# Optimization experiments

Hardware: AMD Instinct MI355X
Metric: run time of the kernel (lower is better)

The kernel has to match this reference:

```python
import jax, jax.numpy as jnp
import numpy as np

EMBED = 1024
HEADS = 16
HEAD_DIM = EMBED // HEADS


def setup_inputs() -> dict:
    key = jax.random.key(0)
    ks = jax.random.split(key, 5)
    x = jax.random.normal(ks[0], (4, 2048, EMBED), dtype=jnp.float32)
    s = 1.0 / np.sqrt(EMBED)
    W_qkv = jax.random.normal(ks[1], (EMBED, 3 * EMBED), dtype=jnp.float32) * s
    b_qkv = jnp.zeros((3 * EMBED,), dtype=jnp.float32)
    W_proj = jax.random.normal(ks[2], (EMBED, EMBED), dtype=jnp.float32) * s
    b_proj = jnp.zeros((EMBED,), dtype=jnp.float32)
    return {"x": x, "W_qkv": W_qkv, "b_qkv": b_qkv, "W_proj": W_proj, "b_proj": b_proj}


def reference(x, W_qkv, b_qkv, W_proj, b_proj):
    B, S, E = x.shape
    scale = 1.0 / np.sqrt(HEAD_DIM)
    qkv = x @ W_qkv + b_qkv                      # [B,S,3E]
    qkv = qkv.reshape(B, S, 3, HEADS, HEAD_DIM)
    q, k, v = qkv[:, :, 0], qkv[:, :, 1], qkv[:, :, 2]   # [B,S,H,D]
    scores = jnp.einsum('bshd,bthd->bhst', q, k) * scale  # [B,H,S,S]
    attn = jax.nn.softmax(scores, axis=-1)
    out = jnp.einsum('bhst,bthd->bshd', attn, v)          # [B,S,H,D]
    out = out.reshape(B, S, E)
    return out @ W_proj + b_proj
```

## Files before the change

kernel.cpp:

```cpp
#include <hip/hip_runtime.h>
#include <math.h>

#define EMBED 1024
#define HEADS 16
#define HD    64
#define SEQ   2048
#define BATCH 4
#define ROWS  (BATCH * SEQ)

typedef _Float16 f16;
typedef __attribute__((ext_vector_type(8))) _Float16 f16x8;
typedef __attribute__((ext_vector_type(4))) _Float16 f16x4;
typedef __attribute__((ext_vector_type(2))) _Float16 f16x2;
typedef __attribute__((ext_vector_type(4))) float    fx4;

typedef __attribute__((address_space(3))) char  lds_char;
typedef __attribute__((address_space(1))) const char glb_char;

#define SCALE_Q 0.18033688011112042f

__global__ __launch_bounds__(256) void prep(const float* __restrict__ x,
                                            f16* __restrict__ x_h,
                                            const float* __restrict__ Wqkv,
                                            f16* __restrict__ Wqt,
                                            const float* __restrict__ Wproj,
                                            f16* __restrict__ Wpt) {
    const int blk = blockIdx.x;
    if (blk < 8192) {
        const int i = (blk * 256 + threadIdx.x) * 4;
        const float4 v = *(const float4*)(x + i);
        f16x4 o = {(f16)v.x, (f16)v.y, (f16)v.z, (f16)v.w};
        *(f16x4*)(x_h + i) = o;
        return;
    }
    __shared__ float t[32][33];
    const float* W;
    f16* Wt;
    int N, bx, by;
    if (blk < 8192 + 3072) {
        const int b2 = blk - 8192;
        W = Wqkv; Wt = Wqt; N = 3072; bx = b2 % 96; by = b2 / 96;
    } else {
        const int b2 = blk - 8192 - 3072;
        W = Wproj; Wt = Wpt; N = 1024; bx = b2 % 32; by = b2 / 32;
    }
    const int tx = threadIdx.x & 31, ty = threadIdx.x >> 5;
    const int k0 = by * 32, n0 = bx * 32;
    #pragma unroll
    for (int i = 0; i < 4; i++)
        t[ty + i * 8][tx] = W[(size_t)(k0 + ty + i * 8) * N + n0 + tx];
    __syncthreads();
    #pragma unroll
    for (int i = 0; i < 4; i++)
        Wt[(size_t)(n0 + ty + i * 8) * 1024 + k0 + tx] = (f16)t[tx][ty + i * 8];
}

template <int MODE>
__global__ __launch_bounds__(256) void gemm_f16k(const f16* __restrict__ A,
                                                 const f16* __restrict__ Bt,
                                                 const float* __restrict__ bias,
                                                 float* __restrict__ Cf,
                                                 f16* __restrict__ qH,
                                                 f16* __restrict__ kH,
                                                 f16* __restrict__ vT,
                                                 int M, int N, int K) {
    __shared__ alignas(16) f16 As[128][64];
    __shared__ alignas(16) f16 Bs[128][64];
    const int tid  = threadIdx.x;
    const int wave = tid >> 6;
    const int lane = tid & 63;
    const int quad = lane >> 4;
    const int l16  = lane & 15;

    const int nwg  = gridDim.x * gridDim.y;
    const int flat = blockIdx.y * gridDim.x + blockIdx.x;
    const int swz  = (flat & 7) * (nwg >> 3) + (flat >> 3);
    const int bx   = swz % gridDim.x;
    const int by   = swz / gridDim.x;
    const int m0   = by * 128;
    const int n0   = bx * 128;
    const int wm   = wave & 1;
    const int wn   = wave >> 1;

    fx4 acc[4][4];
    #pragma unroll
    for (int i = 0; i < 4; i++)
        #pragma unroll
        for (int j = 0; j < 4; j++)
            acc[i][j] = (fx4){0.f, 0.f, 0.f, 0.f};

    lds_char* asb = (lds_char*)&As[0][0];
    lds_char* bsb = (lds_char*)&Bs[0][0];

    const int srow = lane >> 3;
    const int sjl  = ((lane & 7) ^ (srow & 7)) * 8;
    auto STAGE = [&](int k0) {
        #pragma unroll
        for (int it = 0; it < 4; it++) {
            const int g = it * 4 + wave;
            const int r = g * 8 + srow;
            __builtin_amdgcn_global_load_lds(
                (glb_char*)(A + (size_t)(m0 + r) * K + k0 + sjl),
                asb + g * 1024, 16, 0, 0);
            __builtin_amdgcn_global_load_lds(
                (glb_char*)(Bt + (size_t)(n0 + r) * K + k0 + sjl),
                bsb + g * 1024, 16, 0, 0);
        }
    };

    STAGE(0);
    __syncthreads();

    const int NKB = K >> 6;
    for (int kb = 0; kb < NKB; kb++) {
        f16x8 af0[4], af1[4], bf0[4], bf1[4];
        #pragma unroll
        for (int t = 0; t < 4; t++) {
            const int ra = wm * 64 + t * 16 + l16;
            const int rb = wn * 64 + t * 16 + l16;
            af0[t] = *(const f16x8*)&As[ra][((0 + quad) ^ (ra & 7)) * 8];
            af1[t] = *(const f16x8*)&As[ra][((4 + quad) ^ (ra & 7)) * 8];
            bf0[t] = *(const f16x8*)&Bs[rb][((0 + quad) ^ (rb & 7)) * 8];
            bf1[t] = *(const f16x8*)&Bs[rb][((4 + quad) ^ (rb & 7)) * 8];
        }

        #pragma unroll
        for (int i = 0; i < 4; i++)
            #pragma unroll
            for (int j = 0; j < 4; j++)
                acc[i][j] = __builtin_amdgcn_mfma_f32_16x16x32_f16(af0[i], bf0[j], acc[i][j], 0, 0, 0);

        __syncthreads();
        if (kb + 1 < NKB) STAGE((kb + 1) << 6);

        #pragma unroll
        for (int i = 0; i < 4; i++)
            #pragma unroll
            for (int j = 0; j < 4; j++)
                acc[i][j] = __builtin_amdgcn_mfma_f32_16x16x32_f16(af1[i], bf1[j], acc[i][j], 0, 0, 0);

        __syncthreads();
    }

    const int region = n0 >> 10;
    #pragma unroll
    for (int i = 0; i < 4; i++) {
        const int mb = m0 + wm * 64 + i * 16 + quad * 4;
        #pragma unroll
        for (int j = 0; j < 4; j++) {
            const int n  = n0 + wn * 64 + j * 16 + l16;
            const float bn = bias[n];
            #pragma unroll
            for (int r = 0; r < 4; r++) {
                const int m = mb + r;
                const float v = acc[i][j][r] + bn;
                if (MODE == 0) {
                    Cf[(size_t)m * N + n] = v;
                } else {
                    const int b = m >> 11, s = m & 2047;
                    if (region == 0) {
                        qH[(size_t)m * EMBED + n] = (f16)(v * SCALE_Q);
                    } else if (region == 1) {
                        const int np = n - 1024, hh = np >> 6, d = np & 63;
                        kH[(((size_t)(b * 16 + hh) * SEQ + s) << 6) + d] = (f16)v;
                    } else {
                        const int np = n - 2048, hh = np >> 6, d = np & 63;
                        const int sp = (s & ~31) | ((s & 15) << 1) | ((s >> 4) & 1);
                        vT[((size_t)(b * 16 + hh) * HD + d) * SEQ + sp] = (f16)v;
                    }
                }
            }
        }
    }
}

__global__ __launch_bounds__(256, 4) void attn_mfma(const f16* __restrict__ qH,
                                                    const f16* __restrict__ kH,
                                                    const f16* __restrict__ vT,
                                                    f16* __restrict__ ctx) {
    __shared__ alignas(16) f16 Ks[64 * 64];
    __shared__ alignas(16) f16 Vt[64 * 64];
    __shared__ alignas(16) f16 Pl[4][2][16 * 64];

    const int tid  = threadIdx.x;
    const int wave = tid >> 6;
    const int lane = tid & 63;
    const int quad = lane >> 4;
    const int l16  = lane & 15;

    const int bid = (int)blockIdx.x;
    const int swz = (bid & 7) * 128 + (bid >> 3);
    const int qb = swz & 15;
    const int bh = swz >> 4;
    const int h  = bh & 15;
    const int b  = bh >> 4;
    const int q0 = qb * 128 + wave * 32;

    const f16* kB = kH + (size_t)bh * SEQ * HD;
    const f16* vB = vT + (size_t)bh * HD * SEQ;

    f16x8 qf[2][2];
    #pragma unroll
    for (int s = 0; s < 2; s++) {
        const f16* qp = qH + (size_t)(b * SEQ + q0 + s * 16 + l16) * EMBED + h * HD;
        #pragma unroll
        for (int c = 0; c < 2; c++)
            qf[s][c] = *(const f16x8*)(qp + c * 32 + quad * 8);
    }

    fx4 o[2][4];
    fx4 ls[2];
    #pragma unroll
    for (int s = 0; s < 2; s++) {
        ls[s] = (fx4){0.f, 0.f, 0.f, 0.f};
        #pragma unroll
        for (int dc = 0; dc < 4; dc++)
            o[s][dc] = (fx4){0.f, 0.f, 0.f, 0.f};
    }

    f16x8 ones8;
    #pragma unroll
    for (int j = 0; j < 8; j++) ones8[j] = (f16)1.0f;

    lds_char* ksb = (lds_char*)&Ks[0];
    lds_char* vsb = (lds_char*)&Vt[0];

    auto STAGE_K = [&](int kb) {
        #pragma unroll
        for (int it = 0; it < 2; it++) {
            const int g  = wave * 2 + it;
            const int c  = g * 64 + lane;
            const int r  = c >> 3;
            const int jl = (c & 7) ^ (r & 7);
            __builtin_amdgcn_global_load_lds(
                (glb_char*)(kB + (size_t)(kb * 64 + r) * HD + jl * 8),
                ksb + g * 1024, 16, 0, 0);
        }
    };
    auto STAGE_V = [&](int kb) {
        #pragma unroll
        for (int it = 0; it < 2; it++) {
            const int g  = wave * 2 + it;
            const int c  = g * 64 + lane;
            const int r  = c >> 3;
            const int jl = (c & 7) ^ (r & 7);
            __builtin_amdgcn_global_load_lds(
                (glb_char*)(vB + (size_t)r * SEQ + kb * 64 + jl * 8),
                vsb + g * 1024, 16, 0, 0);
        }
    };

    STAGE_K(0);
    STAGE_V(0);
    __syncthreads();

    for (int kb = 0; kb < SEQ / 64; kb++) {
        fx4 st0[4], st1[4];
        __builtin_amdgcn_s_setprio(1);
        #pragma unroll
        for (int t = 0; t < 4; t++) {
            const int row = l16 + 16 * t;
            const f16x8 kt0 = *(const f16x8*)&Ks[(row * 8 + ((0 + quad) ^ (row & 7))) * 8];
            const f16x8 kt1 = *(const f16x8*)&Ks[(row * 8 + ((4 + quad) ^ (row & 7))) * 8];
            fx4 z = {0.f, 0.f, 0.f, 0.f};
            st0[t] = __builtin_amdgcn_mfma_f32_16x16x32_f16(qf[0][0], kt0, z, 0, 0, 0);
            st0[t] = __builtin_amdgcn_mfma_f32_16x16x32_f16(qf[0][1], kt1, st0[t], 0, 0, 0);
            st1[t] = __builtin_amdgcn_mfma_f32_16x16x32_f16(qf[1][0], kt0, z, 0, 0, 0);
            st1[t] = __builtin_amdgcn_mfma_f32_16x16x32_f16(qf[1][1], kt1, st1[t], 0, 0, 0);
        }
        __builtin_amdgcn_s_setprio(0);

        #pragma unroll
        for (int g = 0; g < 2; g++)
            #pragma unroll
            for (int r = 0; r < 4; r++) {
                const int row = quad * 4 + r;
                const int cc  = (g * 4 + (l16 >> 2)) ^ (row & 7);
                {
                    const float pa = __builtin_amdgcn_exp2f(st0[2 * g][r]);
                    const float pb = __builtin_amdgcn_exp2f(st0[2 * g + 1][r]);
                    const f16x2 pk = __builtin_bit_cast(f16x2, __builtin_amdgcn_cvt_pkrtz(pa, pb));
                    *(f16x2*)&Pl[wave][0][row * 64 + cc * 8 + (l16 & 3) * 2] = pk;
                }
                {
                    const float pa = __builtin_amdgcn_exp2f(st1[2 * g][r]);
                    const float pb = __builtin_amdgcn_exp2f(st1[2 * g + 1][r]);
                    const f16x2 pk = __builtin_bit_cast(f16x2, __builtin_amdgcn_cvt_pkrtz(pa, pb));
                    *(f16x2*)&Pl[wave][1][row * 64 + cc * 8 + (l16 & 3) * 2] = pk;
                }
            }

        __syncthreads();
        if (kb + 1 < SEQ / 64) STAGE_K(kb + 1);

        const f16x8 pf00 = *(const f16x8*)&Pl[wave][0][l16 * 64 + ((0 + quad) ^ (l16 & 7)) * 8];
        const f16x8 pf01 = *(const f16x8*)&Pl[wave][0][l16 * 64 + ((4 + quad) ^ (l16 & 7)) * 8];
        const f16x8 pf10 = *(const f16x8*)&Pl[wave][1][l16 * 64 + ((0 + quad) ^ (l16 & 7)) * 8];
        const f16x8 pf11 = *(const f16x8*)&Pl[wave][1][l16 * 64 + ((4 + quad) ^ (l16 & 7)) * 8];
        __builtin_amdgcn_s_setprio(1);
        #pragma unroll
        for (int dc = 0; dc < 4; dc++) {
            const int row = 16 * dc + l16;
            const f16x8 vf0 = *(const f16x8*)&Vt[(row * 8 + ((0 + quad) ^ (row & 7))) * 8];
            const f16x8 vf1 = *(const f16x8*)&Vt[(row * 8 + ((4 + quad) ^ (row & 7))) * 8];
            o[0][dc] = __builtin_amdgcn_mfma_f32_16x16x32_f16(pf00, vf0, o[0][dc], 0, 0, 0);
            o[0][dc] = __builtin_amdgcn_mfma_f32_16x16x32_f16(pf01, vf1, o[0][dc], 0, 0, 0);
            o[1][dc] = __builtin_amdgcn_mfma_f32_16x16x32_f16(pf10, vf0, o[1][dc], 0, 0, 0);
            o[1][dc] = __builtin_amdgcn_mfma_f32_16x16x32_f16(pf11, vf1, o[1][dc], 0, 0, 0);
        }
        ls[0] = __builtin_amdgcn_mfma_f32_16x16x32_f16(pf00, ones8, ls[0], 0, 0, 0);
        ls[0] = __builtin_amdgcn_mfma_f32_16x16x32_f16(pf01, ones8, ls[0], 0, 0, 0);
        ls[1] = __builtin_amdgcn_mfma_f32_16x16x32_f16(pf10, ones8, ls[1], 0, 0, 0);
        ls[1] = __builtin_amdgcn_mfma_f32_16x16x32_f16(pf11, ones8, ls[1], 0, 0, 0);
        __builtin_amdgcn_s_setprio(0);

        __syncthreads();
        if (kb + 1 < SEQ / 64) STAGE_V(kb + 1);
    }

    #pragma unroll
    for (int s = 0; s < 2; s++) {
        #pragma unroll
        for (int r = 0; r < 4; r++) {
            const float inv = 1.0f / ls[s][r];
            const int q = q0 + s * 16 + quad * 4 + r;
            f16* dst = ctx + (size_t)(b * SEQ + q) * EMBED + h * HD;
            #pragma unroll
            for (int dc = 0; dc < 4; dc++)
                dst[dc * 16 + l16] = (f16)(o[s][dc][r] * inv);
        }
    }
}

extern "C" void kernel_launch(void* const* d_in, const int* in_sizes, int n_in,
                              void* d_out, int out_size, void* d_ws, size_t ws_size,
                              hipStream_t stream) {
    const float* x     = (const float*)d_in[0];
    const float* Wqkv  = (const float*)d_in[1];
    const float* bqkv  = (const float*)d_in[2];
    const float* Wproj = (const float*)d_in[3];
    const float* bproj = (const float*)d_in[4];
    float* out = (float*)d_out;

    f16* x_h = (f16*)d_ws;
    f16* qHb = x_h + (size_t)ROWS * EMBED;
    f16* kHb = qHb + (size_t)ROWS * EMBED;
    f16* vTb = kHb + (size_t)ROWS * EMBED;
    f16* ctx = vTb + (size_t)ROWS * EMBED;
    f16* Wqt = ctx + (size_t)ROWS * EMBED;
    f16* Wpt = Wqt + (size_t)3 * EMBED * EMBED;

    prep<<<dim3(12288), dim3(256), 0, stream>>>(x, x_h, Wqkv, Wqt, Wproj, Wpt);

    gemm_f16k<1><<<dim3(3 * EMBED / 128, ROWS / 128), dim3(256), 0, stream>>>(
        x_h, Wqt, bqkv, nullptr, qHb, kHb, vTb, ROWS, 3 * EMBED, EMBED);

    attn_mfma<<<dim3(64 * 16), dim3(256), 0, stream>>>(qHb, kHb, vTb, ctx);

    gemm_f16k<0><<<dim3(EMBED / 128, ROWS / 128), dim3(256), 0, stream>>>(
        ctx, Wpt, bproj, out, nullptr, nullptr, nullptr, ROWS, EMBED, EMBED);
}
```

Baseline: 295.8 us.

## Double-buffer GEMM LDS tiles with vmcnt barriers and stage vT epilogue through LDS

Changes the f16 GEMM main loop to use two LDS buffers per operand. Loads run two k-tiles ahead, and the block synchronises with explicit s_waitcnt/s_barrier sequences and s_setprio around the MFMA block instead of two __syncthreads per iteration. The transposed-V epilogue now writes the tile into swizzled LDS and then issues coalesced 16-byte global stores, replacing scattered 2-byte stores. LDS use per block doubles to 64KB, which may lower occupancy, and the hand-written waitcnt counts must match the number of outstanding loads.

```diff
diff --git a/kernel.cpp b/kernel.cpp
--- a/kernel.cpp
+++ b/kernel.cpp
@@ -18,6 +18,10 @@
 typedef __attribute__((address_space(1))) const char glb_char;
 
 #define SCALE_Q 0.18033688011112042f
+
+#define BAR_LGKM()  asm volatile("s_waitcnt lgkmcnt(0)\n\ts_barrier" ::: "memory")
+#define BAR_VM8()   asm volatile("s_waitcnt vmcnt(8)\n\ts_barrier" ::: "memory")
+#define BAR_VM0()   asm volatile("s_waitcnt vmcnt(0)\n\ts_barrier" ::: "memory")
 
 __global__ __launch_bounds__(256) void prep(const float* __restrict__ x,
                                             f16* __restrict__ x_h,
@@ -64,8 +68,18 @@
                                                  f16* __restrict__ kH,
                                                  f16* __restrict__ vT,
                                                  int M, int N, int K) {
-    __shared__ alignas(16) f16 As[128][64];
-    __shared__ alignas(16) f16 Bs[128][64];
+    constexpr int TEL = 128 * 64;
+    __shared__ alignas(16) f16 smem[4 * TEL];
+
+    f16 (*As0)[64] = (f16(*)[64])(smem);
+    f16 (*As1)[64] = (f16(*)[64])(smem + TEL);
+    f16 (*Bs0)[64] = (f16(*)[64])(smem + 2 * TEL);
+    f16 (*Bs1)[64] = (f16(*)[64])(smem + 3 * TEL);
+    lds_char* a0b = (lds_char*)smem;
+    lds_char* a1b = (lds_char*)smem + 2 * TEL;
+    lds_char* b0b = (lds_char*)smem + 4 * TEL;
+    lds_char* b1b = (lds_char*)smem + 6 * TEL;
+
     const int tid  = threadIdx.x;
     const int wave = tid >> 6;
     const int lane = tid & 63;
@@ -89,12 +103,9 @@
         for (int j = 0; j < 4; j++)
             acc[i][j] = (fx4){0.f, 0.f, 0.f, 0.f};
 
-    lds_char* asb = (lds_char*)&As[0][0];
-    lds_char* bsb = (lds_char*)&Bs[0][0];
-
     const int srow = lane >> 3;
     const int sjl  = ((lane & 7) ^ (srow & 7)) * 8;
-    auto STAGE = [&](int k0) {
+    auto STAGE = [&](lds_char* asb, lds_char* bsb, int k0) {
         #pragma unroll
         for (int it = 0; it < 4; it++) {
             const int g = it * 4 + wave;
@@ -108,41 +119,80 @@
         }
     };
 
-    STAGE(0);
-    __syncthreads();
-
-    const int NKB = K >> 6;
-    for (int kb = 0; kb < NKB; kb++) {
+    const int NT = K >> 6;
+
+    auto ITER = [&](f16 (*As)[64], f16 (*Bs)[64],
+                    lds_char* asb, lds_char* bsb, int t) {
         f16x8 af0[4], af1[4], bf0[4], bf1[4];
         #pragma unroll
-        for (int t = 0; t < 4; t++) {
-            const int ra = wm * 64 + t * 16 + l16;
-            const int rb = wn * 64 + t * 16 + l16;
-            af0[t] = *(const f16x8*)&As[ra][((0 + quad) ^ (ra & 7)) * 8];
-            af1[t] = *(const f16x8*)&As[ra][((4 + quad) ^ (ra & 7)) * 8];
-            bf0[t] = *(const f16x8*)&Bs[rb][((0 + quad) ^ (rb & 7)) * 8];
-            bf1[t] = *(const f16x8*)&Bs[rb][((4 + quad) ^ (rb & 7)) * 8];
-        }
-
+        for (int i = 0; i < 4; i++) {
+            const int ra = wm * 64 + i * 16 + l16;
+            const int rb = wn * 64 + i * 16 + l16;
+            af0[i] = *(const f16x8*)&As[ra][((0 + quad) ^ (ra & 7)) * 8];
+            af1[i] = *(const f16x8*)&As[ra][((4 + quad) ^ (ra & 7)) * 8];
+            bf0[i] = *(const f16x8*)&Bs[rb][((0 + quad) ^ (rb & 7)) * 8];
+            bf1[i] = *(const f16x8*)&Bs[rb][((4 + quad) ^ (rb & 7)) * 8];
+        }
+        BAR_LGKM();
+        const bool more = (t + 2 < NT);
+        if (more) STAGE(asb, bsb, (t + 2) * 64);
+        __builtin_amdgcn_s_setprio(1);
         #pragma unroll
         for (int i = 0; i < 4; i++)
             #pragma unroll
-            for (int j = 0; j < 4; j++)
+            for (int j = 0; j < 4; j++) {
                 acc[i][j] = __builtin_amdgcn_mfma_f32_16x16x32_f16(af0[i], bf0[j], acc[i][j], 0, 0, 0);
-
+                acc[i][j] = __builtin_amdgcn_mfma_f32_16x16x32_f16(af1[i], bf1[j], acc[i][j], 0, 0, 0);
+            }
+        __builtin_amdgcn_s_setprio(0);
+        if (more) BAR_VM8(); else BAR_VM0();
+    };
+
+    STAGE(a0b, b0b, 0);
+    STAGE(a1b, b1b, 64);
+    BAR_VM8();
+
+    for (int t = 0; t < NT; t += 2) {
+        ITER(As0, Bs0, a0b, b0b, t);
+        ITER(As1, Bs1, a1b, b1b, t + 1);
+    }
+
+    const int region = (MODE == 1) ? (n0 >> 10) : 0;
+
+    if (MODE == 1 && region == 2) {
+        const int b  = m0 >> 11;
+        const int s0 = m0 & 2047;
+        #pragma unroll
+        for (int i = 0; i < 4; i++) {
+            #pragma unroll
+            for (int j = 0; j < 4; j++) {
+                const int nloc = wn * 64 + j * 16 + l16;
+                const float bn = bias[n0 + nloc];
+                #pragma unroll
+                for (int r = 0; r < 4; r++) {
+                    const int sloc = wm * 64 + i * 16 + quad * 4 + r;
+                    const int sp   = (sloc & ~31) | ((sloc & 15) << 1) | ((sloc >> 4) & 1);
+                    const int phys = (sp >> 3) ^ (nloc & 15);
+                    smem[nloc * 128 + phys * 8 + (sp & 7)] = (f16)(acc[i][j][r] + bn);
+                }
+            }
+        }
         __syncthreads();
-        if (kb + 1 < NKB) STAGE((kb + 1) << 6);
-
-        #pragma unroll
-        for (int i = 0; i < 4; i++)
-            #pragma unroll
-            for (int j = 0; j < 4; j++)
-                acc[i][j] = __builtin_amdgcn_mfma_f32_16x16x32_f16(af1[i], bf1[j], acc[i][j], 0, 0, 0);
-
-        __syncthreads();
-    }
-
-    const int region = n0 >> 10;
+        const int nl = tid >> 1;
+        const int hf = tid & 1;
+        const int np0 = n0 - 2048;
+        f16* dst = vT + ((size_t)(b * 16 + ((np0 + nl) >> 6)) * HD + (nl & 63)) * SEQ
+                      + s0 + hf * 64;
+        #pragma unroll
+        for (int ch = 0; ch < 8; ch++) {
+            const int lc   = hf * 8 + ch;
+            const int phys = lc ^ (nl & 15);
+            const f16x8 v  = *(const f16x8*)&smem[nl * 128 + phys * 8];
+            *(f16x8*)(dst + ch * 8) = v;
+        }
+        return;
+    }
+
     #pragma unroll
     for (int i = 0; i < 4; i++) {
         const int mb = m0 + wm * 64 + i * 16 + quad * 4;
@@ -160,13 +210,9 @@
                     const int b = m >> 11, s = m & 2047;
                     if (region == 0) {
                         qH[(size_t)m * EMBED + n] = (f16)(v * SCALE_Q);
-                    } else if (region == 1) {
+                    } else {
                         const int np = n - 1024, hh = np >> 6, d = np & 63;
                         kH[(((size_t)(b * 16 + hh) * SEQ + s) << 6) + d] = (f16)v;
-                    } else {
-                        const int np = n - 2048, hh = np >> 6, d = np & 63;
-                        const int sp = (s & ~31) | ((s & 15) << 1) | ((s >> 4) & 1);
-                        vT[((size_t)(b * 16 + hh) * HD + d) * SEQ + sp] = (f16)v;
                     }
                 }
             }
```

Measured after the change: 269.4 us. 8.9% less time.
